# Performance work log

Measured on AMD Instinct MI355X. Metric: run time of the kernel, lower is better.

Reference implementation:

```python
import jax, jax.numpy as jnp
import numpy as np

BN_EPS = 1e-3  # Keras BatchNormalization default epsilon


def setup_inputs() -> dict:
    key = jax.random.key(0)
    ks = jax.random.split(key, 8)
    N, F, H, S, E = 30000, 16, 16, 8, 300000
    return {
        "x": jax.random.normal(ks[0], (N, F), dtype=jnp.float32),
        "e": jax.random.uniform(ks[1], (E, S), dtype=jnp.float32),
        "src": jax.random.randint(ks[2], (E,), 0, N),
        "dst": jax.random.randint(ks[3], (E,), 0, N),
        "Wk": jax.random.normal(ks[4], (S, F * H), dtype=jnp.float32) * 0.1,
        "bk": jnp.zeros((F * H,), dtype=jnp.float32),
        "Wr": jax.random.normal(ks[5], (F, H), dtype=jnp.float32) * 0.1,
        "br": jnp.zeros((H,), dtype=jnp.float32),
        "gamma": jnp.ones((H,), dtype=jnp.float32),
        "beta": jnp.zeros((H,), dtype=jnp.float32),
        "mmean": jnp.zeros((H,), dtype=jnp.float32),
        "mvar": jnp.ones((H,), dtype=jnp.float32),
        "Wd": jax.random.normal(ks[6], (H, 3), dtype=jnp.float32) * 0.1,
        "bd": jnp.zeros((3,), dtype=jnp.float32),
    }


def reference(x, e, src, dst, Wk, bk, Wr, br, gamma, beta, mmean, mvar, Wd, bd):
    N, F = x.shape
    H = Wr.shape[1]
    # ECCConv: per-edge filter generated from edge features -> [E, F, H]
    kernels = (e @ Wk + bk).reshape(e.shape[0], F, H)
    # message: gather source node feats, apply per-edge kernel
    msg = jnp.einsum('ef,efh->eh', x[src], kernels)  # [E, H]
    # scatter-sum aggregate to target nodes
    agg = jax.ops.segment_sum(msg, dst, num_segments=N)  # [N, H]
    h = jax.nn.relu(agg + x @ Wr + br)
    # BatchNormalization (inference: moving stats); Dropout = identity at eval
    h = (h - mmean) / jnp.sqrt(mvar + BN_EPS) * gamma + beta
    pooled = jnp.max(h, axis=0, keepdims=True)  # GlobalMaxPool, single mode -> [1, H]
    return pooled @ Wd + bd  # [1, 3]
```

## Files before the change

kernel.cpp:

```cpp
#include <hip/hip_runtime.h>

#define BN_EPS 1e-3f

typedef float vf4 __attribute__((ext_vector_type(4)));
typedef float f32x4 __attribute__((ext_vector_type(4)));
typedef _Float16 half8v __attribute__((ext_vector_type(8)));

__device__ __forceinline__ unsigned int f2k(float f) {
    unsigned int u = __float_as_uint(f);
    return (u & 0x80000000u) ? ~u : (u | 0x80000000u);
}
__device__ __forceinline__ float k2f(unsigned int u) {
    return __uint_as_float((u & 0x80000000u) ? (u & 0x7FFFFFFFu) : ~u);
}

template <int S, int F, int H>
__global__ void __launch_bounds__(256)
edge_mfma(const float* __restrict__ efeat,
          const int* __restrict__ src,
          const int* __restrict__ dst,
          const float* __restrict__ x,
          const float* __restrict__ Wk,
          const float* __restrict__ bk,
          float* __restrict__ agg,
          int E) {
    const int lane = threadIdx.x & 63;
    const int g = lane >> 4;
    const int er = lane & 15;

    half8v bfr[5];
#pragma unroll
    for (int fr = 0; fr < 5; ++fr) {
#pragma unroll
        for (int j = 0; j < 8; ++j) {
            int k = fr * 32 + g * 8 + j;
            float w = 0.f;
            if (k < S * F) w = Wk[k * H + er];
            else if (k < S * F + F) w = bk[(k - S * F) * H + er];
            bfr[fr][j] = (_Float16)w;
        }
    }

    const int TILES = (E + 15) >> 4;
    int wid = blockIdx.x * (blockDim.x >> 6) + (threadIdx.x >> 6);
    int wstride = gridDim.x * (blockDim.x >> 6);

    for (int t = wid; t < TILES; t += wstride) {
        int e0 = t << 4;
        int eA = min(e0 + er, E - 1);
        int sn = __builtin_nontemporal_load(src + eA);

        const vf4* xp = (const vf4*)(x + (size_t)sn * F + (g & 1) * 8);
        vf4 xa = xp[0], xb = xp[1];
        float xh[8] = {xa.x, xa.y, xa.z, xa.w, xb.x, xb.y, xb.z, xb.w};

        f32x4 acc = {0.f, 0.f, 0.f, 0.f};
#pragma unroll
        for (int fr = 0; fr < 4; ++fr) {
            float es = __builtin_nontemporal_load(
                efeat + (size_t)eA * S + fr * 2 + (g >> 1));
            half8v a;
#pragma unroll
            for (int j = 0; j < 8; ++j) a[j] = (_Float16)(es * xh[j]);
            acc = __builtin_amdgcn_mfma_f32_16x16x32_f16(a, bfr[fr], acc, 0, 0, 0);
        }
        {
            half8v a;
#pragma unroll
            for (int j = 0; j < 8; ++j)
                a[j] = (g < 2) ? (_Float16)xh[j] : (_Float16)0.f;
            acc = __builtin_amdgcn_mfma_f32_16x16x32_f16(a, bfr[4], acc, 0, 0, 0);
        }

#pragma unroll
        for (int r = 0; r < 4; ++r) {
            int ei = e0 + g * 4 + r;
            if (ei < E) {
                int dn = dst[ei];
                unsafeAtomicAdd(&agg[(size_t)dn * H + er], acc[r]);
            }
        }
    }
}

template <int F, int H>
__global__ void __launch_bounds__(256)
base_bn_relu_max(const float* __restrict__ agg,
                 const float* __restrict__ x,
                 const float* __restrict__ Wr,
                 const float* __restrict__ br,
                 const float* __restrict__ gamma,
                 const float* __restrict__ beta,
                 const float* __restrict__ mmean,
                 const float* __restrict__ mvar,
                 unsigned int* __restrict__ pooled_u,
                 int N) {
    __shared__ unsigned int smax[H];
    if (threadIdx.x < H) smax[threadIdx.x] = 0u;
    __syncthreads();

    int i = blockIdx.x * blockDim.x + threadIdx.x;
    int h4 = (i & 3) * 4;
    float best[4] = {-INFINITY, -INFINITY, -INFINITY, -INFINITY};
    if (i < N * 4) {
        int n = i >> 2;
        const vf4* xr = (const vf4*)(x + (size_t)n * F);
        vf4 x0 = xr[0], x1 = xr[1], x2 = xr[2], x3 = xr[3];
        float xf[16] = {x0.x, x0.y, x0.z, x0.w, x1.x, x1.y, x1.z, x1.w,
                        x2.x, x2.y, x2.z, x2.w, x3.x, x3.y, x3.z, x3.w};
        vf4 a = ((const vf4*)agg)[i];
#pragma unroll
        for (int j = 0; j < 4; ++j) {
            int h = h4 + j;
            float base = br[h];
#pragma unroll
            for (int f = 0; f < F; ++f) base += xf[f] * Wr[f * H + h];
            float w = a[j] + base;
            w = w > 0.f ? w : 0.f;
            float s = gamma[h] * rsqrtf(mvar[h] + BN_EPS);
            w = w * s + (beta[h] - mmean[h] * s);
            best[j] = fmaxf(best[j], w);
        }
    }
#pragma unroll
    for (int j = 0; j < 4; ++j) atomicMax(&smax[h4 + j], f2k(best[j]));
    __syncthreads();
    if (threadIdx.x < H) atomicMax(&pooled_u[threadIdx.x], smax[threadIdx.x]);
}

template <int H>
__global__ void final_matvec(const unsigned int* __restrict__ pooled_u,
                             const float* __restrict__ Wd,
                             const float* __restrict__ bd,
                             float* __restrict__ out,
                             int HOUT) {
    int j = threadIdx.x;
    if (j >= HOUT) return;
    float acc = bd[j];
#pragma unroll
    for (int hh = 0; hh < H; ++hh) acc += k2f(pooled_u[hh]) * Wd[hh * HOUT + j];
    out[j] = acc;
}

extern "C" void kernel_launch(void* const* d_in, const int* in_sizes, int n_in,
                              void* d_out, int out_size, void* d_ws, size_t ws_size,
                              hipStream_t stream) {
    const float* x     = (const float*)d_in[0];
    const float* e     = (const float*)d_in[1];
    const int*   src   = (const int*)d_in[2];
    const int*   dst   = (const int*)d_in[3];
    const float* Wk    = (const float*)d_in[4];
    const float* bk    = (const float*)d_in[5];
    const float* Wr    = (const float*)d_in[6];
    const float* br    = (const float*)d_in[7];
    const float* gamma = (const float*)d_in[8];
    const float* beta  = (const float*)d_in[9];
    const float* mmean = (const float*)d_in[10];
    const float* mvar  = (const float*)d_in[11];
    const float* Wd    = (const float*)d_in[12];
    const float* bd    = (const float*)d_in[13];

    constexpr int S = 8, F = 16, H = 16;
    const int E = in_sizes[2];
    const int N = in_sizes[0] / F;
    const int HOUT = in_sizes[13];

    float* agg = (float*)d_ws;
    unsigned int* pooled_u = (unsigned int*)(agg + (size_t)N * H);

    hipMemsetAsync(d_ws, 0, (size_t)N * H * sizeof(float) + H * sizeof(unsigned int),
                   stream);

    const int T = 256;
    int TILES = (E + 15) / 16;
    int eblocks = (TILES + 15) / 16;
    edge_mfma<S, F, H><<<eblocks, T, 0, stream>>>(e, src, dst, x, Wk, bk, agg, E);

    int bblocks = (N * 4 + T - 1) / T;
    base_bn_relu_max<F, H><<<bblocks, T, 0, stream>>>(
        agg, x, Wr, br, gamma, beta, mmean, mvar, pooled_u, N);

    final_matvec<H><<<1, 64, 0, stream>>>(pooled_u, Wd, bd, (float*)d_out, HOUT);
}
```

Baseline: 121.7 us.

## Process two edge tiles per wave without loop, fuse final matvec via last-block counter

The edge kernel drops its grid-stride loop. Each wave now handles exactly two 16-edge tiles, with all loads hoisted up front and two independent MFMA chains interleaved, and a launch-bounds occupancy hint is added. This is meant to raise memory-level parallelism and hide gather latency. The BN/max kernel vectorises the root-weight matvec and absorbs the final dense layer through a last-block-done atomic counter, removing one kernel launch. The cost is a much larger grid, extra registers for the doubled state, and an extra fence and atomic per block.

```diff
diff --git a/kernel.cpp b/kernel.cpp
--- a/kernel.cpp
+++ b/kernel.cpp
@@ -15,7 +15,7 @@
 }
 
 template <int S, int F, int H>
-__global__ void __launch_bounds__(256)
+__global__ void __launch_bounds__(256, 6)
 edge_mfma(const float* __restrict__ efeat,
           const int* __restrict__ src,
           const int* __restrict__ dst,
@@ -42,60 +42,94 @@
     }
 
     const int TILES = (E + 15) >> 4;
-    int wid = blockIdx.x * (blockDim.x >> 6) + (threadIdx.x >> 6);
-    int wstride = gridDim.x * (blockDim.x >> 6);
-
-    for (int t = wid; t < TILES; t += wstride) {
-        int e0 = t << 4;
-        int eA = min(e0 + er, E - 1);
-        int sn = __builtin_nontemporal_load(src + eA);
-
-        const vf4* xp = (const vf4*)(x + (size_t)sn * F + (g & 1) * 8);
-        vf4 xa = xp[0], xb = xp[1];
-        float xh[8] = {xa.x, xa.y, xa.z, xa.w, xb.x, xb.y, xb.z, xb.w};
-
-        f32x4 acc = {0.f, 0.f, 0.f, 0.f};
-#pragma unroll
-        for (int fr = 0; fr < 4; ++fr) {
-            float es = __builtin_nontemporal_load(
-                efeat + (size_t)eA * S + fr * 2 + (g >> 1));
-            half8v a;
-#pragma unroll
-            for (int j = 0; j < 8; ++j) a[j] = (_Float16)(es * xh[j]);
-            acc = __builtin_amdgcn_mfma_f32_16x16x32_f16(a, bfr[fr], acc, 0, 0, 0);
-        }
-        {
-            half8v a;
-#pragma unroll
-            for (int j = 0; j < 8; ++j)
-                a[j] = (g < 2) ? (_Float16)xh[j] : (_Float16)0.f;
-            acc = __builtin_amdgcn_mfma_f32_16x16x32_f16(a, bfr[4], acc, 0, 0, 0);
-        }
-
-#pragma unroll
-        for (int r = 0; r < 4; ++r) {
-            int ei = e0 + g * 4 + r;
-            if (ei < E) {
-                int dn = dst[ei];
-                unsafeAtomicAdd(&agg[(size_t)dn * H + er], acc[r]);
-            }
+    const int wid = blockIdx.x * (blockDim.x >> 6) + (threadIdx.x >> 6);
+    const int t0 = wid * 2;
+    if (t0 >= TILES) return;
+
+    const int e00 = t0 << 4;
+    const int e01 = e00 + 16;
+    const int eA0 = min(e00 + er, E - 1);
+    const int eA1 = min(e01 + er, E - 1);
+
+    int sn0 = __builtin_nontemporal_load(src + eA0);
+    int sn1 = __builtin_nontemporal_load(src + eA1);
+
+    float es0[4], es1[4];
+#pragma unroll
+    for (int fr = 0; fr < 4; ++fr) {
+        int so = fr * 2 + (g >> 1);
+        es0[fr] = __builtin_nontemporal_load(efeat + (size_t)eA0 * S + so);
+        es1[fr] = __builtin_nontemporal_load(efeat + (size_t)eA1 * S + so);
+    }
+
+    const vf4* xp0 = (const vf4*)(x + (size_t)sn0 * F + (g & 1) * 8);
+    const vf4* xp1 = (const vf4*)(x + (size_t)sn1 * F + (g & 1) * 8);
+    vf4 xa0 = xp0[0], xb0 = xp0[1];
+    vf4 xa1 = xp1[0], xb1 = xp1[1];
+    float xh0[8] = {xa0.x, xa0.y, xa0.z, xa0.w, xb0.x, xb0.y, xb0.z, xb0.w};
+    float xh1[8] = {xa1.x, xa1.y, xa1.z, xa1.w, xb1.x, xb1.y, xb1.z, xb1.w};
+
+    f32x4 acc0 = {0.f, 0.f, 0.f, 0.f};
+    f32x4 acc1 = {0.f, 0.f, 0.f, 0.f};
+#pragma unroll
+    for (int fr = 0; fr < 4; ++fr) {
+        half8v a0, a1;
+#pragma unroll
+        for (int j = 0; j < 8; ++j) {
+            a0[j] = (_Float16)(es0[fr] * xh0[j]);
+            a1[j] = (_Float16)(es1[fr] * xh1[j]);
+        }
+        acc0 = __builtin_amdgcn_mfma_f32_16x16x32_f16(a0, bfr[fr], acc0, 0, 0, 0);
+        acc1 = __builtin_amdgcn_mfma_f32_16x16x32_f16(a1, bfr[fr], acc1, 0, 0, 0);
+    }
+    {
+        half8v a0, a1;
+#pragma unroll
+        for (int j = 0; j < 8; ++j) {
+            a0[j] = (g < 2) ? (_Float16)xh0[j] : (_Float16)0.f;
+            a1[j] = (g < 2) ? (_Float16)xh1[j] : (_Float16)0.f;
+        }
+        acc0 = __builtin_amdgcn_mfma_f32_16x16x32_f16(a0, bfr[4], acc0, 0, 0, 0);
+        acc1 = __builtin_amdgcn_mfma_f32_16x16x32_f16(a1, bfr[4], acc1, 0, 0, 0);
+    }
+
+#pragma unroll
+    for (int r = 0; r < 4; ++r) {
+        int ei = e00 + g * 4 + r;
+        if (ei < E) {
+            int dn = dst[ei];
+            unsafeAtomicAdd(&agg[(size_t)dn * H + er], acc0[r]);
+        }
+    }
+#pragma unroll
+    for (int r = 0; r < 4; ++r) {
+        int ei = e01 + g * 4 + r;
+        if (ei < E) {
+            int dn = dst[ei];
+            unsafeAtomicAdd(&agg[(size_t)dn * H + er], acc1[r]);
         }
     }
 }
 
 template <int F, int H>
 __global__ void __launch_bounds__(256)
-base_bn_relu_max(const float* __restrict__ agg,
-                 const float* __restrict__ x,
-                 const float* __restrict__ Wr,
-                 const float* __restrict__ br,
-                 const float* __restrict__ gamma,
-                 const float* __restrict__ beta,
-                 const float* __restrict__ mmean,
-                 const float* __restrict__ mvar,
-                 unsigned int* __restrict__ pooled_u,
-                 int N) {
+bn_relu_max_final(const float* __restrict__ agg,
+                  const float* __restrict__ x,
+                  const float* __restrict__ Wr,
+                  const float* __restrict__ br,
+                  const float* __restrict__ gamma,
+                  const float* __restrict__ beta,
+                  const float* __restrict__ mmean,
+                  const float* __restrict__ mvar,
+                  unsigned int* __restrict__ pooled_u,
+                  unsigned int* __restrict__ counter,
+                  const float* __restrict__ Wd,
+                  const float* __restrict__ bd,
+                  float* __restrict__ out,
+                  int N, int HOUT) {
     __shared__ unsigned int smax[H];
+    __shared__ float pooled_s[H];
+    __shared__ int is_last;
     if (threadIdx.x < H) smax[threadIdx.x] = 0u;
     __syncthreads();
 
@@ -108,14 +142,15 @@
         vf4 x0 = xr[0], x1 = xr[1], x2 = xr[2], x3 = xr[3];
         float xf[16] = {x0.x, x0.y, x0.z, x0.w, x1.x, x1.y, x1.z, x1.w,
                         x2.x, x2.y, x2.z, x2.w, x3.x, x3.y, x3.z, x3.w};
+        vf4 basev = *(const vf4*)(br + h4);
+#pragma unroll
+        for (int f = 0; f < F; ++f)
+            basev += xf[f] * (*(const vf4*)(Wr + f * H + h4));
         vf4 a = ((const vf4*)agg)[i];
 #pragma unroll
         for (int j = 0; j < 4; ++j) {
             int h = h4 + j;
-            float base = br[h];
-#pragma unroll
-            for (int f = 0; f < F; ++f) base += xf[f] * Wr[f * H + h];
-            float w = a[j] + base;
+            float w = a[j] + basev[j];
             w = w > 0.f ? w : 0.f;
             float s = gamma[h] * rsqrtf(mvar[h] + BN_EPS);
             w = w * s + (beta[h] - mmean[h] * s);
@@ -126,20 +161,27 @@
     for (int j = 0; j < 4; ++j) atomicMax(&smax[h4 + j], f2k(best[j]));
     __syncthreads();
     if (threadIdx.x < H) atomicMax(&pooled_u[threadIdx.x], smax[threadIdx.x]);
-}
-
-template <int H>
-__global__ void final_matvec(const unsigned int* __restrict__ pooled_u,
-                             const float* __restrict__ Wd,
-                             const float* __restrict__ bd,
-                             float* __restrict__ out,
-                             int HOUT) {
-    int j = threadIdx.x;
-    if (j >= HOUT) return;
-    float acc = bd[j];
-#pragma unroll
-    for (int hh = 0; hh < H; ++hh) acc += k2f(pooled_u[hh]) * Wd[hh * HOUT + j];
-    out[j] = acc;
+    __syncthreads();
+
+    if (threadIdx.x == 0) {
+        __threadfence();
+        unsigned int old = atomicAdd(counter, 1u);
+        is_last = (old == gridDim.x - 1) ? 1 : 0;
+    }
+    __syncthreads();
+    if (!is_last) return;
+
+    __threadfence();
+    if (threadIdx.x < H)
+        pooled_s[threadIdx.x] = k2f(atomicMax(&pooled_u[threadIdx.x], 0u));
+    __syncthreads();
+    if (threadIdx.x < HOUT) {
+        float acc = bd[threadIdx.x];
+#pragma unroll
+        for (int hh = 0; hh < H; ++hh)
+            acc += pooled_s[hh] * Wd[hh * HOUT + threadIdx.x];
+        out[threadIdx.x] = acc;
+    }
 }
 
 extern "C" void kernel_launch(void* const* d_in, const int* in_sizes, int n_in,
@@ -167,18 +209,20 @@
 
     float* agg = (float*)d_ws;
     unsigned int* pooled_u = (unsigned int*)(agg + (size_t)N * H);
-
-    hipMemsetAsync(d_ws, 0, (size_t)N * H * sizeof(float) + H * sizeof(unsigned int),
+    unsigned int* counter  = pooled_u + H;
+
+    hipMemsetAsync(d_ws, 0,
+                   (size_t)N * H * sizeof(float) + (H + 1) * sizeof(unsigned int),
                    stream);
 
     const int T = 256;
     int TILES = (E + 15) / 16;
-    int eblocks = (TILES + 15) / 16;
+    int waves = (TILES + 1) / 2;
+    int eblocks = (waves + 3) / 4;
     edge_mfma<S, F, H><<<eblocks, T, 0, stream>>>(e, src, dst, x, Wk, bk, agg, E);
 
     int bblocks = (N * 4 + T - 1) / T;
-    base_bn_relu_max<F, H><<<bblocks, T, 0, stream>>>(
-        agg, x, Wr, br, gamma, beta, mmean, mvar, pooled_u, N);
-
-    final_matvec<H><<<1, 64, 0, stream>>>(pooled_u, Wd, bd, (float*)d_out, HOUT);
-}
+    bn_relu_max_final<F, H><<<bblocks, T, 0, stream>>>(
+        agg, x, Wr, br, gamma, beta, mmean, mvar, pooled_u, counter,
+        Wd, bd, (float*)d_out, N, HOUT);
+}
```

New measurement: 140.4 us. 1.15x slower.
